# Optimization experiments

Hardware: AMD Instinct MI355X
Metric: run time of the kernel (lower is better)

Reference implementation:

```python
import jax, jax.numpy as jnp
import numpy as np

K = 5          # top_k periods
KERNEL = 25    # moving-average kernel for series decomposition
D = 64         # d_model / channels
EPS = 1e-5     # BatchNorm eps (torch default)


def setup_inputs() -> dict:
    key = jax.random.key(0)
    k0, k1, k2, k3, k4 = jax.random.split(key, 5)
    B, T = 8, 2048
    x = jax.random.normal(k0, (B, T, D), jnp.float32)
    w1 = jax.random.normal(k1, (D, D, 3, 3), jnp.float32) * 0.05
    w2 = jax.random.normal(k2, (D, D, 3, 3), jnp.float32) * 0.05
    bn1_gamma = jnp.ones((D,), jnp.float32) + 0.1 * jax.random.normal(k3, (D,), jnp.float32)
    bn2_gamma = jnp.ones((D,), jnp.float32) + 0.1 * jax.random.normal(k4, (D,), jnp.float32)
    z = jnp.zeros((D,), jnp.float32)
    o = jnp.ones((D,), jnp.float32)
    return dict(x=x, w1=w1, w2=w2,
                bn1_gamma=bn1_gamma, bn1_beta=z, bn1_mean=z, bn1_var=o,
                bn2_gamma=bn2_gamma, bn2_beta=z, bn2_mean=z, bn2_var=o)


def _moving_avg(x, kernel):
    # AvgPool1d(stride=1, padding=(kernel-1)//2, count_include_pad=False) over time.
    T = x.shape[1]
    pad = (kernel - 1) // 2
    cs = jnp.concatenate([jnp.zeros_like(x[:, :1]), jnp.cumsum(x, axis=1)], axis=1)  # [B,T+1,C]
    t = jnp.arange(T)
    lo = jnp.clip(t - pad, 0, T)          # inclusive window start
    hi = jnp.clip(t + pad + 1, 0, T)      # exclusive window end
    sums = cs[:, hi] - cs[:, lo]
    return sums / (hi - lo).astype(x.dtype)[None, :, None]


def _auto_corr(s, k):
    T = s.shape[1]
    Xf = jnp.fft.rfft(s, axis=1)
    Pm = (Xf * jnp.conj(Xf)).real.mean(axis=-1)          # [B, T//2+1]
    r = jnp.fft.irfft(Pm, n=T, axis=1)                   # [B, T]
    r = r.at[:, 0].set(-jnp.inf)                          # forbid lag 0
    vals, idx = jax.lax.top_k(r, k)                       # [B,k]
    w = jax.nn.softmax(vals, axis=1)
    return idx, w


def _bn(z, gamma, beta, mean, var):
    return (z - mean) * (gamma * jax.lax.rsqrt(var + EPS)) + beta


def _process_one(s_b, p, w1, w2, bn1, bn2):
    # s_b: [T, C]; p: scalar int period.
    # Equivalent to: roll(s_b, -p), reflect-pad time to cyc*p, fold to [C,cyc,p],
    # Conv2dResBlock (3x3 zero-pad convs + eval BN + GELU + residual), unfold, crop to T.
    T, C = s_b.shape
    U = 2 * T - 2                               # static bound: cyc*p <= T+p-1 <= 2T-2
    u = jnp.arange(U)
    cyc = (T + p - 1) // p
    v = jnp.where(u < T, u, 2 * T - 2 - u)      # reflect extension index
    g = s_b[(v + p) % T]                         # [U,C] rolled-by-(-p) then reflect-padded
    r = u // p                                   # grid row (cycle)
    c = u % p                                    # grid col (phase)

    def conv3x3(z, w):
        # zero-padded 3x3 conv on the [cyc, p] grid, expressed on the flat time axis
        out = jnp.zeros_like(z)
        for dr in (-1, 0, 1):
            for dc in (-1, 0, 1):
                valid = (r + dr >= 0) & (r + dr < cyc) & (c + dc >= 0) & (c + dc < p)
                un = jnp.clip(u + dr * p + dc, 0, U - 1)
                zn = jnp.where(valid[:, None], z[un], 0.0)    # [U,C]
                out = out + zn @ w[:, :, dr + 1, dc + 1].T    # [U,Cout]
        return out

    h = _bn(conv3x3(g, w1), *bn1)
    h = jax.nn.gelu(h, approximate=False)
    h = _bn(conv3x3(h, w2), *bn2)
    return (g + h)[:T]                           # residual + unfold-crop


def reference(x, w1, w2, bn1_gamma, bn1_beta, bn1_mean, bn1_var,
              bn2_gamma, bn2_beta, bn2_mean, bn2_var):
    trend = _moving_avg(x, KERNEL)
    s = x - trend                                # seasonal
    idx, w = _auto_corr(s, K)                    # [B,K] periods, weights
    bn1 = (bn1_gamma, bn1_beta, bn1_mean, bn1_var)
    bn2 = (bn2_gamma, bn2_beta, bn2_mean, bn2_var)
    f = lambda sb, p: _process_one(sb, p, w1, w2, bn1, bn2)
    y = jax.vmap(lambda sb, pb: jax.vmap(lambda p: f(sb, p))(pb))(s, idx)  # [B,K,T,C]
    agg = jnp.einsum('bk,bktc->btc', w, y)
    return agg + trend + x
```

## Files before the change

kernel.cpp:

```cpp
#include <hip/hip_runtime.h>
#include <hip/hip_bf16.h>
#include <math.h>

#define TB 8
#define TT 2048
#define TD 64
#define TK 5
#define TPAD 12
#define EPSBN 1e-5f
#define UMAX 4096

#define ROWS1 128
#define BAND1 130
#define LROWS1 390

#define ROWS2 16
#define BAND2 18
#define LROWS2 54
#define SH8   432
#define BUFB  6912

#define ACG 17

typedef __attribute__((ext_vector_type(8))) short short8;
typedef __attribute__((ext_vector_type(4))) float f32x4;

#define OFF_S     0
#define OFF_SBF   1048576
#define OFF_R     1572864
#define OFF_IDX   1581056
#define OFF_W     1581096
#define OFF_WT1   1581136
#define OFF_WT2   1599568
#define OFF_H1    1618000
#define OFF_CAND  6860880
#define OFF_VALS  6860944

__global__ __launch_bounds__(256) void k_trend(const float* __restrict__ x,
                                               float* __restrict__ out, float* __restrict__ s,
                                               __hip_bfloat16* __restrict__ sbf,
                                               const float* __restrict__ w1, const float* __restrict__ w2,
                                               __hip_bfloat16* __restrict__ wt1, __hip_bfloat16* __restrict__ wt2,
                                               float* __restrict__ r, float* __restrict__ vals)
{
    if (blockIdx.x >= 256) {
        int d = (blockIdx.x - 256) * 256 + threadIdx.x;
        if (d < TB * 1024) r[d] = 0.f;
        if (d < TB * 8) vals[d] = 0.f;
        if (d < 36864) {
            int j = d & 7, l = (d >> 3) & 63, nt = (d >> 9) & 3, kb = d >> 11;
            int tap = kb >> 1, half = kb & 1;
            int co = nt * 16 + (l & 15);
            int ci = half * 32 + (l >> 4) * 8 + j;
            int src = (co * 64 + ci) * 9 + tap;
            wt1[d] = __float2bfloat16(w1[src]);
            wt2[d] = __float2bfloat16(w2[src]);
        }
        return;
    }
    int gid = blockIdx.x * 256 + threadIdx.x;
    int c = gid & 63;
    int tblk = (gid >> 6) & 127;
    int b = gid >> 13;
    int t0 = tblk * 16;
    const float* base = x + (size_t)b * TT * TD + c;
    float sum = 0.f;
    for (int tt = t0 - TPAD; tt <= t0 + TPAD; ++tt)
        if (tt >= 0 && tt < TT) sum += base[(size_t)tt * TD];
    size_t o = (size_t)b * TT * TD + (size_t)t0 * TD + c;
    #pragma unroll
    for (int i = 0; i < 16; ++i) {
        int t = t0 + i;
        int lo = t - TPAD; if (lo < 0) lo = 0;
        int hi = t + TPAD; if (hi > TT - 1) hi = TT - 1;
        float tr = sum / (float)(hi - lo + 1);
        float xv = base[(size_t)t * TD];
        out[o] = xv + tr;
        float sv = xv - tr;
        s[o] = sv;
        sbf[o] = __float2bfloat16(sv);
        int addt = t + TPAD + 1, subt = t - TPAD;
        if (addt < TT) sum += base[(size_t)addt * TD];
        if (subt >= 0) sum -= base[(size_t)subt * TD];
        o += TD;
    }
}

__global__ __launch_bounds__(256) void k_ac_mfma(const short* __restrict__ sbf16, float* __restrict__ r)
{
    int id = blockIdx.x;
    int b = id & 7;
    int slot = id >> 3;
    int g = slot % ACG;
    int qq = slot / ACG;
    int d0 = g * 4;
    int t0 = qq * 32;
    const short* sb = sbf16 + (size_t)b * TT * TD;

    __shared__ short Atile[2][1024];
    __shared__ short Btile[6][1024];
    __shared__ float scr[4][16 * 17];

    int tid = threadIdx.x;
    if (tid < 128) {
        int dst = (tid * 16) ^ (((tid >> 3) & 7) << 4);
        *(short8*)((char*)Atile[t0 & 1] + dst) =
            *(const short8*)(sb + (size_t)((t0 & 127) * 1024) + tid * 8);
        #pragma unroll
        for (int j = 0; j < 4; ++j) {
            int xi = t0 + d0 + j;
            *(short8*)((char*)Btile[xi % 6] + dst) =
                *(const short8*)(sb + (size_t)((xi & 127) * 1024) + tid * 8);
        }
    }
    __syncthreads();

    int lane = tid & 63, wv = tid >> 6;
    int fr = lane & 15, kg = lane >> 4;
    int roff0 = (fr * 128 + kg * 16) ^ ((fr & 7) << 4);
    int roff1 = roff0 ^ 64;
    int myD = d0 + wv;

    f32x4 acc = {};
    for (int stp = 0; stp < 32; ++stp) {
        int ti = t0 + stp;
        short8 sA, sB;
        if (tid < 128) {
            sA = *(const short8*)(sb + (size_t)(((ti + 1) & 127) * 1024) + tid * 8);
            sB = *(const short8*)(sb + (size_t)(((ti + d0 + 4) & 127) * 1024) + tid * 8);
        }
        const char* Ab = (const char*)Atile[ti & 1];
        const char* Bb = (const char*)Btile[(ti + myD) % 6];
        short8 a0 = *(const short8*)(Ab + roff0);
        short8 a1 = *(const short8*)(Ab + roff1);
        short8 b0 = *(const short8*)(Bb + roff0);
        short8 b1 = *(const short8*)(Bb + roff1);
        acc = __builtin_amdgcn_mfma_f32_16x16x32_bf16(a0, b0, acc, 0, 0, 0);
        acc = __builtin_amdgcn_mfma_f32_16x16x32_bf16(a1, b1, acc, 0, 0, 0);
        if (tid < 128) {
            int dst = (tid * 16) ^ (((tid >> 3) & 7) << 4);
            *(short8*)((char*)Atile[(ti + 1) & 1] + dst) = sA;
            *(short8*)((char*)Btile[(ti + d0 + 4) % 6] + dst) = sB;
        }
        __syncthreads();
    }

    float* sc = scr[wv];
    #pragma unroll
    for (int q = 0; q < 4; ++q)
        sc[(kg * 4 + q) * 17 + fr] = acc[q];
    __syncthreads();
    if (lane < 31) {
        int d = lane - 15;
        int lag = 16 * myD + d;
        if (lag >= 1 && lag <= 1024) {
            int m0 = d < 0 ? -d : 0;
            int m1 = d < 0 ? 16 : 16 - d;
            float v = 0.f;
            for (int m = m0; m < m1; ++m) v += sc[m * 17 + m + d];
            atomicAdd(&r[(size_t)b * 1024 + (lag - 1)], v * (1.0f / 64.0f));
        }
    }
}

__global__ __launch_bounds__(256) void k_cand(const float* __restrict__ r, int* __restrict__ cand)
{
    int b = blockIdx.x;
    __shared__ float v[1024];
    __shared__ float redv[256]; __shared__ int redi[256];
    for (int i = threadIdx.x; i < 1024; i += 256) v[i] = r[(size_t)b * 1024 + i];
    __syncthreads();
    for (int round = 0; round < 8; ++round) {
        float bv = -INFINITY; int bi = 1 << 30;
        for (int i = threadIdx.x; i < 1024; i += 256) {
            float val = v[i];
            if (val > bv) { bv = val; bi = i; }
        }
        redv[threadIdx.x] = bv; redi[threadIdx.x] = bi;
        __syncthreads();
        for (int off = 128; off; off >>= 1) {
            if (threadIdx.x < off) {
                float ov = redv[threadIdx.x + off]; int oi = redi[threadIdx.x + off];
                float mv = redv[threadIdx.x];       int mi = redi[threadIdx.x];
                if (ov > mv || (ov == mv && oi < mi)) { redv[threadIdx.x] = ov; redi[threadIdx.x] = oi; }
            }
            __syncthreads();
        }
        if (threadIdx.x == 0) {
            int lag = redi[0] + 1;
            cand[b * 8 + round] = lag;
            v[lag - 1] = -INFINITY;
        }
        __syncthreads();
    }
}

__global__ __launch_bounds__(256) void k_rescore(const float* __restrict__ s, const int* __restrict__ cand,
                                                 float* __restrict__ vals)
{
    int ci = blockIdx.x;
    int tq = blockIdx.y;
    int b = blockIdx.z;
    int lag = cand[b * 8 + ci];
    const float* sb = s + (size_t)b * TT * TD;
    int cg = (threadIdx.x & 15) * 4;
    int t0 = tq * 512 + (threadIdx.x >> 4) * 32;
    float acc = 0.f;
    #pragma unroll 8
    for (int t = t0; t < t0 + 32; ++t) {
        const float4 a = *(const float4*)(sb + ((size_t)t << 6) + cg);
        const float4 w = *(const float4*)(sb + ((size_t)((t + lag) & (TT - 1)) << 6) + cg);
        acc = fmaf(a.x, w.x, acc);
        acc = fmaf(a.y, w.y, acc);
        acc = fmaf(a.z, w.z, acc);
        acc = fmaf(a.w, w.w, acc);
    }
    __shared__ float red[256];
    red[threadIdx.x] = acc;
    __syncthreads();
    for (int off = 128; off; off >>= 1) {
        if (threadIdx.x < off) red[threadIdx.x] += red[threadIdx.x + off];
        __syncthreads();
    }
    if (threadIdx.x == 0) atomicAdd(&vals[b * 8 + ci], red[0] * (1.0f / 64.0f));
}

__global__ __launch_bounds__(64) void k_sel(const float* __restrict__ vals, const int* __restrict__ cand,
                                            int* __restrict__ selidx, float* __restrict__ selw)
{
    int b = blockIdx.x;
    if (threadIdx.x != 0) return;
    float vv[8]; int ll[8]; bool used[8];
    #pragma unroll
    for (int i = 0; i < 8; ++i) { vv[i] = vals[b * 8 + i]; ll[i] = cand[b * 8 + i]; used[i] = false; }
    int s_idx[6]; float s_val[6]; int slots = 0;
    while (slots < 5) {
        float bv = -INFINITY; int bi = -1;
        for (int i = 0; i < 8; ++i) {
            if (!used[i] && (vv[i] > bv || (vv[i] == bv && bi >= 0 && ll[i] < ll[bi]))) { bv = vv[i]; bi = i; }
        }
        used[bi] = true;
        s_idx[slots] = ll[bi]; s_val[slots] = bv; slots++;
        if (slots < 5 && ll[bi] < 1024) { s_idx[slots] = 2048 - ll[bi]; s_val[slots] = bv; slots++; }
    }
    float mx = -INFINITY;
    for (int i = 0; i < 5; ++i) mx = fmaxf(mx, s_val[i]);
    float e[5], sum = 0.f;
    for (int i = 0; i < 5; ++i) { e[i] = expf(s_val[i] - mx); sum += e[i]; }
    for (int i = 0; i < 5; ++i) { selidx[b * TK + i] = s_idx[i]; selw[b * TK + i] = e[i] / sum; }
}

__global__ __launch_bounds__(256) void k_mm1(
    const short* __restrict__ s_bf, const short* __restrict__ wtp,
    const float* __restrict__ g1, const float* __restrict__ b1,
    const float* __restrict__ m1, const float* __restrict__ v1,
    const int* __restrict__ sel, __hip_bfloat16* __restrict__ h1)
{
    int b = blockIdx.z, k = blockIdx.y;
    int p = sel[b * TK + k];
    int cyc = (TT + p - 1) / p;
    int U = cyc * p;
    int u0 = blockIdx.x * ROWS1;
    if (u0 >= U) return;
    __shared__ short As[LROWS1 * 64];

    const short* sb = s_bf + (size_t)b * TT * TD;
    for (int q = threadIdx.x; q < LROWS1 * 8; q += 256) {
        int row = q >> 3, ch = (q & 7) * 8;
        int band = row / BAND1, i = row - band * BAND1;
        int w = u0 + (band - 1) * p - 1 + i;
        int wc = min(max(w, 0), 2 * TT - 2);
        int v = (wc < TT) ? wc : (2 * TT - 2 - wc);
        int sr = (v + p) & (TT - 1);
        short8 d = *(const short8*)(sb + (size_t)sr * TD + ch);
        int off = (row * 128 + ch * 2) ^ ((row & 7) << 4);
        *(short8*)((char*)As + off) = d;
    }
    __syncthreads();

    int lane = threadIdx.x & 63;
    int wv = threadIdx.x >> 6;
    int lr = lane & 15;
    int kg = lane >> 4;
    int lu[2]; bool inU[2], topf[2], botf[2], leftf[2], rightf[2];
    #pragma unroll
    for (int rs = 0; rs < 2; ++rs) {
        lu[rs] = wv * 32 + rs * 16 + lr;
        int u = u0 + lu[rs];
        inU[rs] = (u < U);
        int r = u / p, c = u - r * p;
        topf[rs] = (r == 0); botf[rs] = (r == cyc - 1);
        leftf[rs] = (c == 0); rightf[rs] = (c == p - 1);
    }

    f32x4 acc[2][4] = {};
    short8 zero = {};
    #pragma unroll
    for (int kb = 0; kb < 18; ++kb) {
        const int tap = kb >> 1, half = kb & 1;
        const int dr = tap / 3 - 1, dc = tap % 3 - 1;
        short8 a[2];
        #pragma unroll
        for (int rs = 0; rs < 2; ++rs) {
            int ldsrow = (dr + 1) * BAND1 + lu[rs] + 1 + dc;
            int off = (ldsrow * 128 + half * 64 + kg * 16) ^ ((ldsrow & 7) << 4);
            a[rs] = *(const short8*)((const char*)As + off);
            bool valid = inU[rs]
                       && !(dr == -1 && topf[rs]) && !(dr == 1 && botf[rs])
                       && !(dc == -1 && leftf[rs]) && !(dc == 1 && rightf[rs]);
            if (!valid) a[rs] = zero;
        }
        #pragma unroll
        for (int nt = 0; nt < 4; ++nt) {
            short8 bq = *(const short8*)(wtp + (size_t)(kb * 4 + nt) * 512 + lane * 8);
            #pragma unroll
            for (int rs = 0; rs < 2; ++rs)
                acc[rs][nt] = __builtin_amdgcn_mfma_f32_16x16x32_bf16(a[rs], bq, acc[rs][nt], 0, 0, 0);
        }
    }
    __hip_bfloat16* ho = h1 + (size_t)(b * TK + k) * (UMAX * TD);
    #pragma unroll
    for (int nt = 0; nt < 4; ++nt) {
        int co = nt * 16 + lr;
        float scale = g1[co] * rsqrtf(v1[co] + EPSBN);
        float bias = b1[co] - m1[co] * scale;
        #pragma unroll
        for (int rs = 0; rs < 2; ++rs) {
            int ub = u0 + wv * 32 + rs * 16 + kg * 4;
            #pragma unroll
            for (int q = 0; q < 4; ++q) {
                int uo = ub + q;
                if (uo < U) {
                    float z = acc[rs][nt][q] * scale + bias;
                    float ge = 0.5f * z * (1.0f + erff(z * 0.70710678118654752f));
                    ho[(size_t)uo * TD + co] = __float2bfloat16(ge);
                }
            }
        }
    }
}

__global__ __launch_bounds__(256) void k_mm2f(
    const short* __restrict__ h1, const short* __restrict__ wtp,
    const float* __restrict__ s,
    const float* __restrict__ g2, const float* __restrict__ b2,
    const float* __restrict__ m2, const float* __restrict__ v2,
    const int* __restrict__ sel, const float* __restrict__ selw,
    float* __restrict__ out)
{
    int b = blockIdx.y;
    int u0 = blockIdx.x * ROWS2;
    int tid = threadIdx.x;
    __shared__ short As[2 * LROWS2 * 64];

    int lane = tid & 63, wv = tid >> 6, lr = lane & 15, kg = lane >> 4;
    int u = u0 + lr;
    const float* sb = s + (size_t)b * TT * TD;

    f32x4 accT = {};
    float gacc[4] = {0.f, 0.f, 0.f, 0.f};
    short8 sreg[2];
    short8 zero = {};

    {
        int p0 = sel[b * TK];
        const short* hb = h1 + (size_t)(b * TK) * (UMAX * TD);
        #pragma unroll
        for (int it = 0; it < 2; ++it) {
            int q = tid + it * 256;
            if (q < SH8) {
                int row = q >> 3, ch = (q & 7) * 8;
                int band = row / BAND2, i = row - band * BAND2;
                int w = u0 + (band - 1) * p0 - 1 + i;
                int wc = min(max(w, 0), UMAX - 1);
                short8 d = *(const short8*)(hb + (size_t)wc * TD + ch);
                int off = (row * 128 + ch * 2) ^ ((row & 7) << 4);
                *(short8*)((char*)As + off) = d;
            }
        }
    }
    __syncthreads();

    for (int k = 0; k < TK; ++k) {
        int p = sel[b * TK + k];
        float wk = selw[b * TK + k];
        int cyc = (TT + p - 1) / p;
        if (k < TK - 1) {
            int pn = sel[b * TK + k + 1];
            const short* hb = h1 + (size_t)(b * TK + k + 1) * (UMAX * TD);
            #pragma unroll
            for (int it = 0; it < 2; ++it) {
                int q = tid + it * 256;
                if (q < SH8) {
                    int row = q >> 3, ch = (q & 7) * 8;
                    int band = row / BAND2, i = row - band * BAND2;
                    int w = u0 + (band - 1) * pn - 1 + i;
                    int wc = min(max(w, 0), UMAX - 1);
                    sreg[it] = *(const short8*)(hb + (size_t)wc * TD + ch);
                }
            }
        }
        const char* Ab = (const char*)As + (k & 1) * BUFB;
        int r = u / p, c = u - r * p;
        bool topf = (r == 0), botf = (r == cyc - 1), leftf = (c == 0), rightf = (c == p - 1);
        f32x4 accP[2] = {};
        #pragma unroll
        for (int kb = 0; kb < 18; ++kb) {
            const int tap = kb >> 1, half = kb & 1;
            const int dr = tap / 3 - 1, dc = tap % 3 - 1;
            int ldsrow = (dr + 1) * BAND2 + lr + 1 + dc;
            int off = (ldsrow * 128 + half * 64 + kg * 16) ^ ((ldsrow & 7) << 4);
            short8 a = *(const short8*)(Ab + off);
            bool valid = !(dr == -1 && topf) && !(dr == 1 && botf)
                       && !(dc == -1 && leftf) && !(dc == 1 && rightf);
            if (!valid) a = zero;
            short8 bq = *(const short8*)(wtp + (size_t)(kb * 4 + wv) * 512 + lane * 8);
            accP[kb & 1] = __builtin_amdgcn_mfma_f32_16x16x32_bf16(a, bq, accP[kb & 1], 0, 0, 0);
        }
        #pragma unroll
        for (int e = 0; e < 4; ++e) accT[e] += wk * (accP[0][e] + accP[1][e]);
        #pragma unroll
        for (int q = 0; q < 4; ++q) {
            int uo = u0 + kg * 4 + q;
            int sr = (uo + p) & (TT - 1);
            gacc[q] = fmaf(wk, sb[(size_t)sr * TD + wv * 16 + lr], gacc[q]);
        }
        __syncthreads();
        if (k < TK - 1) {
            char* Aw = (char*)As + ((k + 1) & 1) * BUFB;
            #pragma unroll
            for (int it = 0; it < 2; ++it) {
                int q = tid + it * 256;
                if (q < SH8) {
                    int row = q >> 3, ch = (q & 7) * 8;
                    int off = (row * 128 + ch * 2) ^ ((row & 7) << 4);
                    *(short8*)(Aw + off) = sreg[it];
                }
            }
            __syncthreads();
        }
    }

    float* ob = out + (size_t)b * TT * TD;
    int co = wv * 16 + lr;
    float scale = g2[co] * rsqrtf(v2[co] + EPSBN);
    float bias = b2[co] - m2[co] * scale;
    #pragma unroll
    for (int q = 0; q < 4; ++q) {
        int uo = u0 + kg * 4 + q;
        size_t idx = (size_t)uo * TD + co;
        ob[idx] = ob[idx] + gacc[q] + scale * accT[q] + bias;
    }
}

extern "C" void kernel_launch(void* const* d_in, const int* in_sizes, int n_in,
                              void* d_out, int out_size, void* d_ws, size_t ws_size,
                              hipStream_t stream)
{
    const float* x  = (const float*)d_in[0];
    const float* w1 = (const float*)d_in[1];
    const float* w2 = (const float*)d_in[2];
    const float* g1 = (const float*)d_in[3];
    const float* b1 = (const float*)d_in[4];
    const float* m1 = (const float*)d_in[5];
    const float* v1 = (const float*)d_in[6];
    const float* g2 = (const float*)d_in[7];
    const float* b2 = (const float*)d_in[8];
    const float* m2 = (const float*)d_in[9];
    const float* v2 = (const float*)d_in[10];

    float* ws    = (float*)d_ws;
    float* s     = ws + OFF_S;
    __hip_bfloat16* sbf = (__hip_bfloat16*)(ws + OFF_SBF);
    float* r     = ws + OFF_R;
    int*   sel   = (int*)(ws + OFF_IDX);
    float* selw  = ws + OFF_W;
    __hip_bfloat16* wt1 = (__hip_bfloat16*)(ws + OFF_WT1);
    __hip_bfloat16* wt2 = (__hip_bfloat16*)(ws + OFF_WT2);
    __hip_bfloat16* h1  = (__hip_bfloat16*)(ws + OFF_H1);
    int*   cand  = (int*)(ws + OFF_CAND);
    float* vals  = ws + OFF_VALS;
    float* out   = (float*)d_out;

    k_trend   <<<dim3(400),         dim3(256), 0, stream>>>(x, out, s, sbf, w1, w2, wt1, wt2, r, vals);
    k_ac_mfma <<<dim3(544),         dim3(256), 0, stream>>>((const short*)sbf, r);
    k_cand    <<<dim3(TB),          dim3(256), 0, stream>>>(r, cand);
    k_rescore <<<dim3(8, 4, TB),    dim3(256), 0, stream>>>(s, cand, vals);
    k_sel     <<<dim3(TB),          dim3(64),  0, stream>>>(vals, cand, sel, selw);
    k_mm1     <<<dim3(32, TK, TB),  dim3(256), 0, stream>>>((const short*)sbf, (const short*)wt1,
                                                            g1, b1, m1, v1, sel, h1);
    k_mm2f    <<<dim3(128, TB),     dim3(256), 0, stream>>>((const short*)h1, (const short*)wt2, s,
                                                            g2, b2, m2, v2, sel, selw, out);
}
```

Measured before the change: 114.2 us.

## Fuse candidate top-k, rescore and selection into one kernel; vectorize trend

Merges the candidate-lag search, exact rescore and softmax selection kernels into a single 512-thread block per batch. The argmax uses wave shuffles and each wave rescores one candidate, which removes two launches, the vals zeroing and the global atomics. The trend kernel now handles four channels per thread with float4 loads and stores, so it needs fewer blocks. The rescore now runs on only 8 blocks, with each wave walking the full sequence, so that step loses parallelism on a critical-path stage.

```diff
diff --git a/kernel.cpp b/kernel.cpp
--- a/kernel.cpp
+++ b/kernel.cpp
@@ -33,20 +33,17 @@
 #define OFF_WT1   1581136
 #define OFF_WT2   1599568
 #define OFF_H1    1618000
-#define OFF_CAND  6860880
-#define OFF_VALS  6860944
 
 __global__ __launch_bounds__(256) void k_trend(const float* __restrict__ x,
                                                float* __restrict__ out, float* __restrict__ s,
                                                __hip_bfloat16* __restrict__ sbf,
                                                const float* __restrict__ w1, const float* __restrict__ w2,
                                                __hip_bfloat16* __restrict__ wt1, __hip_bfloat16* __restrict__ wt2,
-                                               float* __restrict__ r, float* __restrict__ vals)
-{
-    if (blockIdx.x >= 256) {
-        int d = (blockIdx.x - 256) * 256 + threadIdx.x;
+                                               float* __restrict__ r)
+{
+    if (blockIdx.x >= 64) {
+        int d = (blockIdx.x - 64) * 256 + threadIdx.x;
         if (d < TB * 1024) r[d] = 0.f;
-        if (d < TB * 8) vals[d] = 0.f;
         if (d < 36864) {
             int j = d & 7, l = (d >> 3) & 63, nt = (d >> 9) & 3, kb = d >> 11;
             int tap = kb >> 1, half = kb & 1;
@@ -59,29 +56,47 @@
         return;
     }
     int gid = blockIdx.x * 256 + threadIdx.x;
-    int c = gid & 63;
-    int tblk = (gid >> 6) & 127;
-    int b = gid >> 13;
+    int cq = (gid & 15) * 4;
+    int tblk = (gid >> 4) & 127;
+    int b = gid >> 11;
     int t0 = tblk * 16;
-    const float* base = x + (size_t)b * TT * TD + c;
-    float sum = 0.f;
-    for (int tt = t0 - TPAD; tt <= t0 + TPAD; ++tt)
-        if (tt >= 0 && tt < TT) sum += base[(size_t)tt * TD];
-    size_t o = (size_t)b * TT * TD + (size_t)t0 * TD + c;
+    const float* base = x + (size_t)b * TT * TD + cq;
+    float4 sum = make_float4(0.f, 0.f, 0.f, 0.f);
+    for (int tt = t0 - TPAD; tt <= t0 + TPAD; ++tt) {
+        if (tt >= 0 && tt < TT) {
+            float4 v = *(const float4*)(base + (size_t)tt * TD);
+            sum.x += v.x; sum.y += v.y; sum.z += v.z; sum.w += v.w;
+        }
+    }
+    size_t o = (size_t)b * TT * TD + (size_t)t0 * TD + cq;
     #pragma unroll
     for (int i = 0; i < 16; ++i) {
         int t = t0 + i;
         int lo = t - TPAD; if (lo < 0) lo = 0;
         int hi = t + TPAD; if (hi > TT - 1) hi = TT - 1;
-        float tr = sum / (float)(hi - lo + 1);
-        float xv = base[(size_t)t * TD];
-        out[o] = xv + tr;
-        float sv = xv - tr;
-        s[o] = sv;
-        sbf[o] = __float2bfloat16(sv);
+        float inv = 1.0f / (float)(hi - lo + 1);
+        float4 xv = *(const float4*)(base + (size_t)t * TD);
+        float4 tr = make_float4(sum.x * inv, sum.y * inv, sum.z * inv, sum.w * inv);
+        float4 ov = make_float4(xv.x + tr.x, xv.y + tr.y, xv.z + tr.z, xv.w + tr.w);
+        float4 sv = make_float4(xv.x - tr.x, xv.y - tr.y, xv.z - tr.z, xv.w - tr.w);
+        *(float4*)(out + o) = ov;
+        *(float4*)(s + o) = sv;
+        ushort4 us;
+        __hip_bfloat16 tb;
+        tb = __float2bfloat16(sv.x); us.x = *(unsigned short*)&tb;
+        tb = __float2bfloat16(sv.y); us.y = *(unsigned short*)&tb;
+        tb = __float2bfloat16(sv.z); us.z = *(unsigned short*)&tb;
+        tb = __float2bfloat16(sv.w); us.w = *(unsigned short*)&tb;
+        *(ushort4*)((unsigned short*)sbf + o) = us;
         int addt = t + TPAD + 1, subt = t - TPAD;
-        if (addt < TT) sum += base[(size_t)addt * TD];
-        if (subt >= 0) sum -= base[(size_t)subt * TD];
+        if (addt < TT) {
+            float4 v = *(const float4*)(base + (size_t)addt * TD);
+            sum.x += v.x; sum.y += v.y; sum.z += v.z; sum.w += v.w;
+        }
+        if (subt >= 0) {
+            float4 v = *(const float4*)(base + (size_t)subt * TD);
+            sum.x -= v.x; sum.y -= v.y; sum.z -= v.z; sum.w -= v.w;
+        }
         o += TD;
     }
 }
@@ -163,91 +178,80 @@
     }
 }
 
-__global__ __launch_bounds__(256) void k_cand(const float* __restrict__ r, int* __restrict__ cand)
+__global__ __launch_bounds__(512) void k_select(const float* __restrict__ r, const float* __restrict__ s,
+                                                int* __restrict__ selidx, float* __restrict__ selw)
 {
     int b = blockIdx.x;
+    int tid = threadIdx.x;
+    int lane = tid & 63, wv = tid >> 6;
     __shared__ float v[1024];
-    __shared__ float redv[256]; __shared__ int redi[256];
-    for (int i = threadIdx.x; i < 1024; i += 256) v[i] = r[(size_t)b * 1024 + i];
+    __shared__ float wredv[8]; __shared__ int wredi[8];
+    __shared__ int candl[8]; __shared__ float valsl[8];
+    for (int i = tid; i < 1024; i += 512) v[i] = r[(size_t)b * 1024 + i];
     __syncthreads();
     for (int round = 0; round < 8; ++round) {
-        float bv = -INFINITY; int bi = 1 << 30;
-        for (int i = threadIdx.x; i < 1024; i += 256) {
-            float val = v[i];
-            if (val > bv) { bv = val; bi = i; }
-        }
-        redv[threadIdx.x] = bv; redi[threadIdx.x] = bi;
+        float bv = v[tid]; int bi = tid;
+        {
+            float v2 = v[tid + 512];
+            if (v2 > bv) { bv = v2; bi = tid + 512; }
+        }
+        #pragma unroll
+        for (int m = 32; m; m >>= 1) {
+            float ov = __shfl_xor(bv, m); int oi = __shfl_xor(bi, m);
+            if (ov > bv || (ov == bv && oi < bi)) { bv = ov; bi = oi; }
+        }
+        if (lane == 0) { wredv[wv] = bv; wredi[wv] = bi; }
         __syncthreads();
-        for (int off = 128; off; off >>= 1) {
-            if (threadIdx.x < off) {
-                float ov = redv[threadIdx.x + off]; int oi = redi[threadIdx.x + off];
-                float mv = redv[threadIdx.x];       int mi = redi[threadIdx.x];
-                if (ov > mv || (ov == mv && oi < mi)) { redv[threadIdx.x] = ov; redi[threadIdx.x] = oi; }
-            }
-            __syncthreads();
-        }
-        if (threadIdx.x == 0) {
-            int lag = redi[0] + 1;
-            cand[b * 8 + round] = lag;
-            v[lag - 1] = -INFINITY;
+        if (tid == 0) {
+            float mv = wredv[0]; int mi = wredi[0];
+            for (int i = 1; i < 8; ++i) {
+                if (wredv[i] > mv || (wredv[i] == mv && wredi[i] < mi)) { mv = wredv[i]; mi = wredi[i]; }
+            }
+            candl[round] = mi + 1;
+            v[mi] = -INFINITY;
         }
         __syncthreads();
     }
-}
-
-__global__ __launch_bounds__(256) void k_rescore(const float* __restrict__ s, const int* __restrict__ cand,
-                                                 float* __restrict__ vals)
-{
-    int ci = blockIdx.x;
-    int tq = blockIdx.y;
-    int b = blockIdx.z;
-    int lag = cand[b * 8 + ci];
-    const float* sb = s + (size_t)b * TT * TD;
-    int cg = (threadIdx.x & 15) * 4;
-    int t0 = tq * 512 + (threadIdx.x >> 4) * 32;
-    float acc = 0.f;
-    #pragma unroll 8
-    for (int t = t0; t < t0 + 32; ++t) {
-        const float4 a = *(const float4*)(sb + ((size_t)t << 6) + cg);
-        const float4 w = *(const float4*)(sb + ((size_t)((t + lag) & (TT - 1)) << 6) + cg);
-        acc = fmaf(a.x, w.x, acc);
-        acc = fmaf(a.y, w.y, acc);
-        acc = fmaf(a.z, w.z, acc);
-        acc = fmaf(a.w, w.w, acc);
-    }
-    __shared__ float red[256];
-    red[threadIdx.x] = acc;
-    __syncthreads();
-    for (int off = 128; off; off >>= 1) {
-        if (threadIdx.x < off) red[threadIdx.x] += red[threadIdx.x + off];
-        __syncthreads();
-    }
-    if (threadIdx.x == 0) atomicAdd(&vals[b * 8 + ci], red[0] * (1.0f / 64.0f));
-}
-
-__global__ __launch_bounds__(64) void k_sel(const float* __restrict__ vals, const int* __restrict__ cand,
-                                            int* __restrict__ selidx, float* __restrict__ selw)
-{
-    int b = blockIdx.x;
-    if (threadIdx.x != 0) return;
-    float vv[8]; int ll[8]; bool used[8];
-    #pragma unroll
-    for (int i = 0; i < 8; ++i) { vv[i] = vals[b * 8 + i]; ll[i] = cand[b * 8 + i]; used[i] = false; }
-    int s_idx[6]; float s_val[6]; int slots = 0;
-    while (slots < 5) {
-        float bv = -INFINITY; int bi = -1;
-        for (int i = 0; i < 8; ++i) {
-            if (!used[i] && (vv[i] > bv || (vv[i] == bv && bi >= 0 && ll[i] < ll[bi]))) { bv = vv[i]; bi = i; }
-        }
-        used[bi] = true;
-        s_idx[slots] = ll[bi]; s_val[slots] = bv; slots++;
-        if (slots < 5 && ll[bi] < 1024) { s_idx[slots] = 2048 - ll[bi]; s_val[slots] = bv; slots++; }
-    }
-    float mx = -INFINITY;
-    for (int i = 0; i < 5; ++i) mx = fmaxf(mx, s_val[i]);
-    float e[5], sum = 0.f;
-    for (int i = 0; i < 5; ++i) { e[i] = expf(s_val[i] - mx); sum += e[i]; }
-    for (int i = 0; i < 5; ++i) { selidx[b * TK + i] = s_idx[i]; selw[b * TK + i] = e[i] / sum; }
+    {
+        int lag = candl[wv];
+        const float* sb = s + (size_t)b * TT * TD;
+        int cg = (lane & 15) * 4;
+        int t0 = (lane >> 4) * 512;
+        float acc = 0.f;
+        #pragma unroll 8
+        for (int t = t0; t < t0 + 512; ++t) {
+            const float4 a = *(const float4*)(sb + ((size_t)t << 6) + cg);
+            const float4 w = *(const float4*)(sb + ((size_t)((t + lag) & (TT - 1)) << 6) + cg);
+            acc = fmaf(a.x, w.x, acc);
+            acc = fmaf(a.y, w.y, acc);
+            acc = fmaf(a.z, w.z, acc);
+            acc = fmaf(a.w, w.w, acc);
+        }
+        #pragma unroll
+        for (int m = 32; m; m >>= 1) acc += __shfl_xor(acc, m);
+        if (lane == 0) valsl[wv] = acc * (1.0f / 64.0f);
+    }
+    __syncthreads();
+    if (tid == 0) {
+        float vv[8]; int ll[8]; bool used[8];
+        #pragma unroll
+        for (int i = 0; i < 8; ++i) { vv[i] = valsl[i]; ll[i] = candl[i]; used[i] = false; }
+        int s_idx[6]; float s_val[6]; int slots = 0;
+        while (slots < 5) {
+            float bv = -INFINITY; int bi = -1;
+            for (int i = 0; i < 8; ++i) {
+                if (!used[i] && (vv[i] > bv || (vv[i] == bv && bi >= 0 && ll[i] < ll[bi]))) { bv = vv[i]; bi = i; }
+            }
+            used[bi] = true;
+            s_idx[slots] = ll[bi]; s_val[slots] = bv; slots++;
+            if (slots < 5 && ll[bi] < 1024) { s_idx[slots] = 2048 - ll[bi]; s_val[slots] = bv; slots++; }
+        }
+        float mx = -INFINITY;
+        for (int i = 0; i < 5; ++i) mx = fmaxf(mx, s_val[i]);
+        float e[5], sum = 0.f;
+        for (int i = 0; i < 5; ++i) { e[i] = expf(s_val[i] - mx); sum += e[i]; }
+        for (int i = 0; i < 5; ++i) { selidx[b * TK + i] = s_idx[i]; selw[b * TK + i] = e[i] / sum; }
+    }
 }
 
 __global__ __launch_bounds__(256) void k_mm1(
@@ -478,15 +482,11 @@
     __hip_bfloat16* wt1 = (__hip_bfloat16*)(ws + OFF_WT1);
     __hip_bfloat16* wt2 = (__hip_bfloat16*)(ws + OFF_WT2);
     __hip_bfloat16* h1  = (__hip_bfloat16*)(ws + OFF_H1);
-    int*   cand  = (int*)(ws + OFF_CAND);
-    float* vals  = ws + OFF_VALS;
     float* out   = (float*)d_out;
 
-    k_trend   <<<dim3(400),         dim3(256), 0, stream>>>(x, out, s, sbf, w1, w2, wt1, wt2, r, vals);
+    k_trend   <<<dim3(208),         dim3(256), 0, stream>>>(x, out, s, sbf, w1, w2, wt1, wt2, r);
     k_ac_mfma <<<dim3(544),         dim3(256), 0, stream>>>((const short*)sbf, r);
-    k_cand    <<<dim3(TB),          dim3(256), 0, stream>>>(r, cand);
-    k_rescore <<<dim3(8, 4, TB),    dim3(256), 0, stream>>>(s, cand, vals);
-    k_sel     <<<dim3(TB),          dim3(64),  0, stream>>>(vals, cand, sel, selw);
+    k_select  <<<dim3(TB),          dim3(512), 0, stream>>>(r, s, sel, selw);
     k_mm1     <<<dim3(32, TK, TB),  dim3(256), 0, stream>>>((const short*)sbf, (const short*)wt1,
                                                             g1, b1, m1, v1, sel, h1);
     k_mm2f    <<<dim3(128, TB),     dim3(256), 0, stream>>>((const short*)h1, (const short*)wt2, s,
```

Measured after the change: 232.9 us. 104% more time.
